# Kernel tuning notes

Measured on AMD Instinct MI355X. Metric: run time of the kernel, lower is better.

## Reference

```python
import jax, jax.numpy as jnp
import numpy as np

OUT = 7          # output_size
SR = 2           # sampling_ratio
IMG = 512.0      # image size (512, 512)
CANON_SCALE = 224.0
CANON_LVL = 4.0
LVL_MIN, LVL_MAX = 2, 6  # strides 4..64


def roi_align_level(feat, rois, scale):
    """torchvision roi_align (aligned=False) for all rois on one level.
    feat: [B,C,H,W], rois: [B,N,4] in image coords. Returns [B,N,C,7,7]."""
    B, C, H, W = feat.shape
    N = rois.shape[1]
    x1 = rois[..., 0] * scale
    y1 = rois[..., 1] * scale
    x2 = rois[..., 2] * scale
    y2 = rois[..., 3] * scale
    roi_w = jnp.maximum(x2 - x1, 1.0)
    roi_h = jnp.maximum(y2 - y1, 1.0)
    bin_w = roi_w / OUT
    bin_h = roi_h / OUT
    # 14 sample coordinates per axis: 7 bins x 2 samples, offset (i+0.5)/2 within bin
    grid = (jnp.arange(OUT, dtype=feat.dtype)[:, None]
            + (jnp.arange(SR, dtype=feat.dtype)[None, :] + 0.5) / SR).reshape(-1)  # [14]
    py = y1[..., None] + grid * bin_h[..., None]   # [B,N,14]
    px = x1[..., None] + grid * bin_w[..., None]   # [B,N,14]
    yy = py[..., :, None]                          # [B,N,14,1]
    xx = px[..., None, :]                          # [B,N,1,14]
    valid = (yy >= -1.0) & (yy <= H) & (xx >= -1.0) & (xx <= W)  # [B,N,14,14]
    y = jnp.clip(yy, 0.0, H - 1)
    x = jnp.clip(xx, 0.0, W - 1)
    y0f = jnp.floor(y)
    x0f = jnp.floor(x)
    ly = y - y0f   # [B,N,14,1]
    lx = x - x0f   # [B,N,1,14]
    y0 = y0f.astype(jnp.int32)
    x0 = x0f.astype(jnp.int32)
    y1i = jnp.minimum(y0 + 1, H - 1)
    x1i = jnp.minimum(x0 + 1, W - 1)

    flat = feat.reshape(B, C, H * W)

    def gather(yi, xi):
        idx = (yi * W + xi).reshape(B, -1)                     # [B, N*14*14]
        g = jax.vmap(lambda f, i: f[:, i])(flat, idx)          # [B, C, N*14*14]
        return g.reshape(B, C, N, SR * OUT, SR * OUT)

    w00 = ((1 - ly) * (1 - lx))[:, None]  # [B,1,N,14,14]
    w01 = ((1 - ly) * lx)[:, None]
    w10 = (ly * (1 - lx))[:, None]
    w11 = (ly * lx)[:, None]
    val = (gather(y0, x0) * w00 + gather(y0, x1i) * w01
           + gather(y1i, x0) * w10 + gather(y1i, x1i) * w11)
    val = val * valid[:, None].astype(feat.dtype)
    # average the SRxSR samples within each bin
    out = val.reshape(B, C, N, OUT, SR, OUT, SR).mean(axis=(4, 6))  # [B,C,N,7,7]
    return out.transpose(0, 2, 1, 3, 4)  # [B,N,C,7,7]


def setup_inputs() -> dict:
    key = jax.random.key(0)
    ks = jax.random.split(key, 6)
    B, C, N = 4, 256, 256
    feats = {}
    for lvl, hw in enumerate([128, 64, 32, 16, 8]):
        feats[f"feat{lvl}"] = jax.random.normal(ks[lvl], (B, C, hw, hw), dtype=jnp.float32)
    # random boxes inside the 512x512 image with x2>x1, y2>y1
    xy = jax.random.uniform(ks[5], (B, N, 2, 2), minval=0.0, maxval=IMG)
    lo = xy.min(axis=2)
    hi = xy.max(axis=2)
    rois = jnp.concatenate([lo, hi], axis=-1)  # [B,N,4] = (x1,y1,x2,y2)
    feats["rois"] = rois
    return feats


def reference(feat0, feat1, feat2, feat3, feat4, rois):
    B, N = rois.shape[0], rois.shape[1]
    feats = [feat0, feat1, feat2, feat3, feat4]
    scales = [0.25, 0.125, 0.0625, 0.03125, 0.015625]  # inferred from 128..8 vs 512
    # FPN level assignment (torchvision LevelMapper)
    area = (rois[..., 2] - rois[..., 0]) * (rois[..., 3] - rois[..., 1])
    lvl = jnp.floor(CANON_LVL + jnp.log2(jnp.sqrt(area) / CANON_SCALE + 1e-6))
    lvl = (jnp.clip(lvl, LVL_MIN, LVL_MAX) - LVL_MIN).astype(jnp.int32)  # [B,N] in 0..4
    # pool every roi on every level, then select its assigned level
    stacked = jnp.stack([roi_align_level(f, rois, s) for f, s in zip(feats, scales)],
                        axis=2)  # [B,N,5,C,7,7]
    sel = jnp.take_along_axis(stacked,
                              lvl[:, :, None, None, None, None].astype(jnp.int32),
                              axis=2)[:, :, 0]  # [B,N,C,7,7]
    B_, N_, C, _, _ = sel.shape
    return sel.reshape(B_ * N_, C, OUT, OUT)
```

## Files before the change

### kernel.cpp

```cpp
#include <hip/hip_runtime.h>

#define OUT 7
#define NB 4
#define NC 256
#define NN 256
#define EPR (NC * OUT * OUT)

typedef float nfloat4 __attribute__((ext_vector_type(4)));

__global__ __launch_bounds__(256) void transpose_cl(
    const float* __restrict__ in, float* __restrict__ outT, int P)
{
    __shared__ float tile[32][33];
    const int p0 = blockIdx.x * 32;
    const int c0 = blockIdx.y * 32;
    const int b  = blockIdx.z;
    const int tx = threadIdx.x;
    const int ty = threadIdx.y;

    const float* src = in + ((size_t)(b * NC + c0 + ty)) * P + p0 + tx * 4;
    nfloat4 v = *(const nfloat4*)src;
    tile[ty][tx * 4 + 0] = v.x;
    tile[ty][tx * 4 + 1] = v.y;
    tile[ty][tx * 4 + 2] = v.z;
    tile[ty][tx * 4 + 3] = v.w;
    __syncthreads();

    nfloat4 w;
    w.x = tile[4 * tx + 0][ty];
    w.y = tile[4 * tx + 1][ty];
    w.z = tile[4 * tx + 2][ty];
    w.w = tile[4 * tx + 3][ty];
    float* dst = outT + ((size_t)b * P + p0 + ty) * NC + c0 + tx * 4;
    *(nfloat4*)dst = w;
}

__global__ __launch_bounds__(256) void msroi_fast(
    const float* __restrict__ T, const float* __restrict__ rois,
    float* __restrict__ out)
{
    const int roi = blockIdx.x;
    const int c   = threadIdx.x;

    __shared__ float s_wyt[14], s_wyb[14], s_wxl[14], s_wxr[14];
    __shared__ int   s_yr0[14], s_yr1[14], s_x0[14], s_x1[14];
    __shared__ int   s_lvl;
    __shared__ __align__(16) float s_out[EPR];

    if (c < 28) {
        const float rx1 = rois[roi * 4 + 0];
        const float ry1 = rois[roi * 4 + 1];
        const float rx2 = rois[roi * 4 + 2];
        const float ry2 = rois[roi * 4 + 3];

        float area = (rx2 - rx1) * (ry2 - ry1);
        float lf = floorf(4.0f + log2f(sqrtf(area) / 224.0f + 1e-6f));
        lf = fminf(fmaxf(lf, 2.0f), 6.0f);
        int lvl = (int)lf - 2;
        if (c == 0) s_lvl = lvl;

        float scale = 1.0f / (float)(4 << lvl);
        int   W     = 128 >> lvl;

        float x1 = rx1 * scale, y1 = ry1 * scale;
        float x2 = rx2 * scale, y2 = ry2 * scale;
        float rw = fmaxf(x2 - x1, 1.0f);
        float rh = fmaxf(y2 - y1, 1.0f);
        float bw = rw / (float)OUT;
        float bh = rh / (float)OUT;

        bool isx = (c >= 14);
        int  g   = isx ? c - 14 : c;
        float gv = ((float)g + 0.5f) * 0.5f;
        float p  = isx ? (x1 + gv * bw) : (y1 + gv * bh);

        float v = (p >= -1.0f && p <= (float)W) ? 1.0f : 0.0f;
        float pc  = fminf(fmaxf(p, 0.0f), (float)(W - 1));
        float p0f = floorf(pc);
        int   p0  = (int)p0f;
        int   p1  = min(p0 + 1, W - 1);
        float l   = pc - p0f;

        if (isx) {
            s_x0[g] = p0; s_x1[g] = p1;
            s_wxl[g] = v * (1.0f - l); s_wxr[g] = v * l;
        } else {
            s_yr0[g] = p0 * W; s_yr1[g] = p1 * W;
            s_wyt[g] = v * (1.0f - l); s_wyb[g] = v * l;
        }
    }
    __syncthreads();

    const int lvl = s_lvl;
    const int W   = 128 >> lvl;
    const int POS = W * W;
    const int off_tab[5] = {0, 16777216, 20971520, 22020096, 22282240};
    const int b = roi >> 8;
    const float* base = T + (size_t)off_tab[lvl] + (size_t)b * POS * NC + c;

    for (int oy = 0; oy < OUT; ++oy) {
        const int gy0 = oy * 2, gy1 = gy0 + 1;
        const float wt0 = s_wyt[gy0], wb0 = s_wyb[gy0];
        const float wt1 = s_wyt[gy1], wb1 = s_wyb[gy1];
        const int r00 = s_yr0[gy0], r01 = s_yr1[gy0];
        const int r10 = s_yr0[gy1], r11 = s_yr1[gy1];
        #pragma unroll
        for (int ox = 0; ox < OUT; ++ox) {
            const int gx0 = ox * 2, gx1 = gx0 + 1;
            const float wl0 = s_wxl[gx0], wr0 = s_wxr[gx0];
            const float wl1 = s_wxl[gx1], wr1 = s_wxr[gx1];
            const int x00 = s_x0[gx0], x01 = s_x1[gx0];
            const int x10 = s_x0[gx1], x11 = s_x1[gx1];

            float acc;
            acc  = wt0 * (wl0 * base[(r00 + x00) << 8] + wr0 * base[(r00 + x01) << 8])
                 + wb0 * (wl0 * base[(r01 + x00) << 8] + wr0 * base[(r01 + x01) << 8]);
            acc += wt0 * (wl1 * base[(r00 + x10) << 8] + wr1 * base[(r00 + x11) << 8])
                 + wb0 * (wl1 * base[(r01 + x10) << 8] + wr1 * base[(r01 + x11) << 8]);
            acc += wt1 * (wl0 * base[(r10 + x00) << 8] + wr0 * base[(r10 + x01) << 8])
                 + wb1 * (wl0 * base[(r11 + x00) << 8] + wr0 * base[(r11 + x01) << 8]);
            acc += wt1 * (wl1 * base[(r10 + x10) << 8] + wr1 * base[(r10 + x11) << 8])
                 + wb1 * (wl1 * base[(r11 + x10) << 8] + wr1 * base[(r11 + x11) << 8]);

            s_out[c * 49 + oy * 7 + ox] = acc * 0.25f;
        }
    }
    __syncthreads();

    float* ob = out + (size_t)roi * EPR;
    #pragma unroll
    for (int k = 0; k < 12; ++k) {
        const int f = (c + (k << 8)) << 2;
        nfloat4 v = *(const nfloat4*)&s_out[f];
        __builtin_nontemporal_store(v, (nfloat4*)&ob[f]);
    }
    if (c < 64) {
        const int f = (c + 3072) << 2;
        nfloat4 v = *(const nfloat4*)&s_out[f];
        __builtin_nontemporal_store(v, (nfloat4*)&ob[f]);
    }
}

__global__ __launch_bounds__(256) void msroi_kernel(
    const float* __restrict__ f0, const float* __restrict__ f1,
    const float* __restrict__ f2, const float* __restrict__ f3,
    const float* __restrict__ f4, const float* __restrict__ rois,
    float* __restrict__ out)
{
    const int roi = blockIdx.y;
    const int tid = threadIdx.x;

    __shared__ float s_wyt[14], s_wyb[14];
    __shared__ float s_wxl[14], s_wxr[14];
    __shared__ int   s_oy0[14], s_oy1[14];
    __shared__ int   s_x0[14],  s_x1[14];
    __shared__ int   s_lvl;

    if (tid < 28) {
        const float rx1 = rois[roi * 4 + 0];
        const float ry1 = rois[roi * 4 + 1];
        const float rx2 = rois[roi * 4 + 2];
        const float ry2 = rois[roi * 4 + 3];

        float area = (rx2 - rx1) * (ry2 - ry1);
        float lf = floorf(4.0f + log2f(sqrtf(area) / 224.0f + 1e-6f));
        lf = fminf(fmaxf(lf, 2.0f), 6.0f);
        int lvl = (int)lf - 2;
        if (tid == 0) s_lvl = lvl;

        float scale = 1.0f / (float)(4 << lvl);
        int   HW    = 128 >> lvl;

        float x1 = rx1 * scale, y1 = ry1 * scale;
        float x2 = rx2 * scale, y2 = ry2 * scale;
        float rw = fmaxf(x2 - x1, 1.0f);
        float rh = fmaxf(y2 - y1, 1.0f);
        float bw = rw / (float)OUT;
        float bh = rh / (float)OUT;

        bool isx = (tid >= 14);
        int  g   = isx ? tid - 14 : tid;
        float gv = ((float)g + 0.5f) * 0.5f;
        float p  = isx ? (x1 + gv * bw) : (y1 + gv * bh);

        float v = (p >= -1.0f && p <= (float)HW) ? 1.0f : 0.0f;
        float pc  = fminf(fmaxf(p, 0.0f), (float)(HW - 1));
        float p0f = floorf(pc);
        int   p0  = (int)p0f;
        int   p1  = min(p0 + 1, HW - 1);
        float l   = pc - p0f;

        if (isx) {
            s_x0[g] = p0; s_x1[g] = p1;
            s_wxl[g] = v * (1.0f - l); s_wxr[g] = v * l;
        } else {
            s_oy0[g] = p0 * HW; s_oy1[g] = p1 * HW;
            s_wyt[g] = v * (1.0f - l); s_wyb[g] = v * l;
        }
    }
    __syncthreads();

    const int lvl = s_lvl;
    const int HW  = 128 >> lvl;
    const int HW2 = HW * HW;
    const float* f = (lvl == 0) ? f0 : (lvl == 1) ? f1 : (lvl == 2) ? f2
                     : (lvl == 3) ? f3 : f4;
    const int b = roi >> 8;

    const int e0 = blockIdx.x * 512 + tid;

    float acc[2];
    #pragma unroll
    for (int k = 0; k < 2; ++k) {
        const int e  = e0 + k * 256;
        const int ec = (e < EPR) ? e : 0;
        const int c  = ec / 49;
        const int s  = ec - 49 * c;
        const int oy = s / 7;
        const int ox = s - 7 * oy;

        const float* fp = f + (size_t)(b * NC + c) * (size_t)HW2;

        float a = 0.0f;
        #pragma unroll
        for (int iy = 0; iy < 2; ++iy) {
            const int gy = oy * 2 + iy;
            const float wt = s_wyt[gy], wb = s_wyb[gy];
            const int   o0 = s_oy0[gy], o1 = s_oy1[gy];
            #pragma unroll
            for (int ix = 0; ix < 2; ++ix) {
                const int gx = ox * 2 + ix;
                const float wl = s_wxl[gx], wr = s_wxr[gx];
                const int   x0 = s_x0[gx],  x1i = s_x1[gx];
                const float v00 = fp[o0 + x0];
                const float v01 = fp[o0 + x1i];
                const float v10 = fp[o1 + x0];
                const float v11 = fp[o1 + x1i];
                a += (wt * wl) * v00 + (wt * wr) * v01
                   + (wb * wl) * v10 + (wb * wr) * v11;
            }
        }
        acc[k] = a * 0.25f;
    }

    #pragma unroll
    for (int k = 0; k < 2; ++k) {
        const int e = e0 + k * 256;
        if (e < EPR)
            __builtin_nontemporal_store(acc[k], &out[(size_t)roi * EPR + e]);
    }
}

extern "C" void kernel_launch(void* const* d_in, const int* in_sizes, int n_in,
                              void* d_out, int out_size, void* d_ws, size_t ws_size,
                              hipStream_t stream) {
    const float* f[5] = {(const float*)d_in[0], (const float*)d_in[1],
                         (const float*)d_in[2], (const float*)d_in[3],
                         (const float*)d_in[4]};
    const float* rois = (const float*)d_in[5];
    float* out = (float*)d_out;

    const size_t need = 22347776ull * 4ull;
    if (ws_size >= need) {
        float* T = (float*)d_ws;
        const int P[5]   = {16384, 4096, 1024, 256, 64};
        const int off[5] = {0, 16777216, 20971520, 22020096, 22282240};
        for (int l = 0; l < 5; ++l) {
            dim3 g(P[l] / 32, NC / 32, NB);
            dim3 blk(8, 32);
            transpose_cl<<<g, blk, 0, stream>>>(f[l], T + off[l], P[l]);
        }
        msroi_fast<<<dim3(NB * NN), dim3(256), 0, stream>>>(T, rois, out);
    } else {
        dim3 grid((EPR + 511) / 512, NB * NN);
        dim3 block(256);
        msroi_kernel<<<grid, block, 0, stream>>>(f[0], f[1], f[2], f[3], f[4],
                                                 rois, out);
    }
}
```

Measured before the change: 200.3 us.

## Fuse per-level transposes into one launch and split ROI pooling across channel chunks

The five per-level channel-last transpose launches are merged into one kernel that finds its level and tile from a flattened block index, removing four launches and the tail gaps between them. The pooling kernel now runs 4 blocks per ROI, each covering 64 channels, with the 49 output bins split across four thread groups. This shrinks shared memory per block from the full 256x49 tile to 64x49 and asks for 6 blocks per CU, to raise occupancy and hide gather latency. In exchange, each block recomputes the ROI sampling tables, and gathers now cover 64 contiguous channels (256 bytes) rather than 256.

```diff
diff --git a/kernel.cpp b/kernel.cpp
--- a/kernel.cpp
+++ b/kernel.cpp
@@ -8,17 +8,31 @@
 
 typedef float nfloat4 __attribute__((ext_vector_type(4)));
 
-__global__ __launch_bounds__(256) void transpose_cl(
-    const float* __restrict__ in, float* __restrict__ outT, int P)
+__global__ __launch_bounds__(256) void transpose_all(
+    const float* __restrict__ f0, const float* __restrict__ f1,
+    const float* __restrict__ f2, const float* __restrict__ f3,
+    const float* __restrict__ f4, float* __restrict__ T)
 {
     __shared__ float tile[32][33];
-    const int p0 = blockIdx.x * 32;
-    const int c0 = blockIdx.y * 32;
-    const int b  = blockIdx.z;
-    const int tx = threadIdx.x;
-    const int ty = threadIdx.y;
-
-    const float* src = in + ((size_t)(b * NC + c0 + ty)) * P + p0 + tx * 4;
+    const int bx = blockIdx.x;
+
+    const float* in; float* outp; int P, t, shp;
+    if (bx < 16384)      { in = f0; outp = T;            P = 16384; t = bx;         shp = 9; }
+    else if (bx < 20480) { in = f1; outp = T + 16777216; P = 4096;  t = bx - 16384; shp = 7; }
+    else if (bx < 21504) { in = f2; outp = T + 20971520; P = 1024;  t = bx - 20480; shp = 5; }
+    else if (bx < 21760) { in = f3; outp = T + 22020096; P = 256;   t = bx - 21504; shp = 3; }
+    else                 { in = f4; outp = T + 22282240; P = 64;    t = bx - 21760; shp = 1; }
+
+    const int pt   = t & ((1 << shp) - 1);
+    const int rest = t >> shp;
+    const int ct   = rest & 7;
+    const int b    = rest >> 3;
+    const int p0   = pt << 5;
+    const int c0   = ct << 5;
+    const int tx   = threadIdx.x & 7;
+    const int ty   = threadIdx.x >> 3;
+
+    const float* src = in + ((size_t)((b << 8) + c0 + ty)) * P + p0 + (tx << 2);
     nfloat4 v = *(const nfloat4*)src;
     tile[ty][tx * 4 + 0] = v.x;
     tile[ty][tx * 4 + 1] = v.y;
@@ -31,23 +45,24 @@
     w.y = tile[4 * tx + 1][ty];
     w.z = tile[4 * tx + 2][ty];
     w.w = tile[4 * tx + 3][ty];
-    float* dst = outT + ((size_t)b * P + p0 + ty) * NC + c0 + tx * 4;
+    float* dst = outp + ((size_t)b * P + p0 + ty) * NC + c0 + (tx << 2);
     *(nfloat4*)dst = w;
 }
 
-__global__ __launch_bounds__(256) void msroi_fast(
+__global__ __launch_bounds__(256, 6) void msroi_fast(
     const float* __restrict__ T, const float* __restrict__ rois,
     float* __restrict__ out)
 {
-    const int roi = blockIdx.x;
-    const int c   = threadIdx.x;
+    const int roi   = blockIdx.y;
+    const int chunk = blockIdx.x;
+    const int tid   = threadIdx.x;
 
     __shared__ float s_wyt[14], s_wyb[14], s_wxl[14], s_wxr[14];
     __shared__ int   s_yr0[14], s_yr1[14], s_x0[14], s_x1[14];
     __shared__ int   s_lvl;
-    __shared__ __align__(16) float s_out[EPR];
-
-    if (c < 28) {
+    __shared__ __align__(16) float s_out[64 * 49];
+
+    if (tid < 28) {
         const float rx1 = rois[roi * 4 + 0];
         const float ry1 = rois[roi * 4 + 1];
         const float rx2 = rois[roi * 4 + 2];
@@ -57,7 +72,7 @@
         float lf = floorf(4.0f + log2f(sqrtf(area) / 224.0f + 1e-6f));
         lf = fminf(fmaxf(lf, 2.0f), 6.0f);
         int lvl = (int)lf - 2;
-        if (c == 0) s_lvl = lvl;
+        if (tid == 0) s_lvl = lvl;
 
         float scale = 1.0f / (float)(4 << lvl);
         int   W     = 128 >> lvl;
@@ -69,8 +84,8 @@
         float bw = rw / (float)OUT;
         float bh = rh / (float)OUT;
 
-        bool isx = (c >= 14);
-        int  g   = isx ? c - 14 : c;
+        bool isx = (tid >= 14);
+        int  g   = isx ? tid - 14 : tid;
         float gv = ((float)g + 0.5f) * 0.5f;
         float p  = isx ? (x1 + gv * bw) : (y1 + gv * bh);
 
@@ -96,48 +111,54 @@
     const int POS = W * W;
     const int off_tab[5] = {0, 16777216, 20971520, 22020096, 22282240};
     const int b = roi >> 8;
-    const float* base = T + (size_t)off_tab[lvl] + (size_t)b * POS * NC + c;
-
-    for (int oy = 0; oy < OUT; ++oy) {
+    const int c = tid & 63;
+    const int q = tid >> 6;
+    const float* base = T + (size_t)off_tab[lvl]
+                          + (size_t)b * POS * NC + (chunk << 6) + c;
+
+    const int pstart = (q * 49) >> 2;
+    const int pend   = ((q + 1) * 49) >> 2;
+
+    for (int pos = pstart; pos < pend; ++pos) {
+        const int oy = pos / 7;
+        const int ox = pos - oy * 7;
         const int gy0 = oy * 2, gy1 = gy0 + 1;
+        const int gx0 = ox * 2, gx1 = gx0 + 1;
+
         const float wt0 = s_wyt[gy0], wb0 = s_wyb[gy0];
         const float wt1 = s_wyt[gy1], wb1 = s_wyb[gy1];
         const int r00 = s_yr0[gy0], r01 = s_yr1[gy0];
         const int r10 = s_yr0[gy1], r11 = s_yr1[gy1];
-        #pragma unroll
-        for (int ox = 0; ox < OUT; ++ox) {
-            const int gx0 = ox * 2, gx1 = gx0 + 1;
-            const float wl0 = s_wxl[gx0], wr0 = s_wxr[gx0];
-            const float wl1 = s_wxl[gx1], wr1 = s_wxr[gx1];
-            const int x00 = s_x0[gx0], x01 = s_x1[gx0];
-            const int x10 = s_x0[gx1], x11 = s_x1[gx1];
-
-            float acc;
-            acc  = wt0 * (wl0 * base[(r00 + x00) << 8] + wr0 * base[(r00 + x01) << 8])
-                 + wb0 * (wl0 * base[(r01 + x00) << 8] + wr0 * base[(r01 + x01) << 8]);
-            acc += wt0 * (wl1 * base[(r00 + x10) << 8] + wr1 * base[(r00 + x11) << 8])
-                 + wb0 * (wl1 * base[(r01 + x10) << 8] + wr1 * base[(r01 + x11) << 8]);
-            acc += wt1 * (wl0 * base[(r10 + x00) << 8] + wr0 * base[(r10 + x01) << 8])
-                 + wb1 * (wl0 * base[(r11 + x00) << 8] + wr0 * base[(r11 + x01) << 8]);
-            acc += wt1 * (wl1 * base[(r10 + x10) << 8] + wr1 * base[(r10 + x11) << 8])
-                 + wb1 * (wl1 * base[(r11 + x10) << 8] + wr1 * base[(r11 + x11) << 8]);
-
-            s_out[c * 49 + oy * 7 + ox] = acc * 0.25f;
-        }
-    }
-    __syncthreads();
-
-    float* ob = out + (size_t)roi * EPR;
+        const float wl0 = s_wxl[gx0], wr0 = s_wxr[gx0];
+        const float wl1 = s_wxl[gx1], wr1 = s_wxr[gx1];
+        const int x00 = s_x0[gx0], x01 = s_x1[gx0];
+        const int x10 = s_x0[gx1], x11 = s_x1[gx1];
+
+        float acc;
+        acc  = wt0 * (wl0 * base[(r00 + x00) << 8] + wr0 * base[(r00 + x01) << 8])
+             + wb0 * (wl0 * base[(r01 + x00) << 8] + wr0 * base[(r01 + x01) << 8]);
+        acc += wt0 * (wl1 * base[(r00 + x10) << 8] + wr1 * base[(r00 + x11) << 8])
+             + wb0 * (wl1 * base[(r01 + x10) << 8] + wr1 * base[(r01 + x11) << 8]);
+        acc += wt1 * (wl0 * base[(r10 + x00) << 8] + wr0 * base[(r10 + x01) << 8])
+             + wb1 * (wl0 * base[(r11 + x00) << 8] + wr0 * base[(r11 + x01) << 8]);
+        acc += wt1 * (wl1 * base[(r10 + x10) << 8] + wr1 * base[(r10 + x11) << 8])
+             + wb1 * (wl1 * base[(r11 + x10) << 8] + wr1 * base[(r11 + x11) << 8]);
+
+        s_out[c * 49 + pos] = acc * 0.25f;
+    }
+    __syncthreads();
+
+    float* ob = out + (size_t)roi * EPR + (chunk << 6) * 49;
     #pragma unroll
-    for (int k = 0; k < 12; ++k) {
-        const int f = (c + (k << 8)) << 2;
-        nfloat4 v = *(const nfloat4*)&s_out[f];
-        __builtin_nontemporal_store(v, (nfloat4*)&ob[f]);
-    }
-    if (c < 64) {
-        const int f = (c + 3072) << 2;
-        nfloat4 v = *(const nfloat4*)&s_out[f];
-        __builtin_nontemporal_store(v, (nfloat4*)&ob[f]);
+    for (int k = 0; k < 3; ++k) {
+        const int i = tid + (k << 8);
+        nfloat4 v = *(const nfloat4*)&s_out[i << 2];
+        __builtin_nontemporal_store(v, (nfloat4*)&ob[i << 2]);
+    }
+    if (tid < 16) {
+        const int i = tid + 768;
+        nfloat4 v = *(const nfloat4*)&s_out[i << 2];
+        __builtin_nontemporal_store(v, (nfloat4*)&ob[i << 2]);
     }
 }
 
@@ -254,27 +275,22 @@
 extern "C" void kernel_launch(void* const* d_in, const int* in_sizes, int n_in,
                               void* d_out, int out_size, void* d_ws, size_t ws_size,
                               hipStream_t stream) {
-    const float* f[5] = {(const float*)d_in[0], (const float*)d_in[1],
-                         (const float*)d_in[2], (const float*)d_in[3],
-                         (const float*)d_in[4]};
+    const float* f0   = (const float*)d_in[0];
+    const float* f1   = (const float*)d_in[1];
+    const float* f2   = (const float*)d_in[2];
+    const float* f3   = (const float*)d_in[3];
+    const float* f4   = (const float*)d_in[4];
     const float* rois = (const float*)d_in[5];
     float* out = (float*)d_out;
 
     const size_t need = 22347776ull * 4ull;
     if (ws_size >= need) {
         float* T = (float*)d_ws;
-        const int P[5]   = {16384, 4096, 1024, 256, 64};
-        const int off[5] = {0, 16777216, 20971520, 22020096, 22282240};
-        for (int l = 0; l < 5; ++l) {
-            dim3 g(P[l] / 32, NC / 32, NB);
-            dim3 blk(8, 32);
-            transpose_cl<<<g, blk, 0, stream>>>(f[l], T + off[l], P[l]);
-        }
-        msroi_fast<<<dim3(NB * NN), dim3(256), 0, stream>>>(T, rois, out);
+        transpose_all<<<dim3(21824), dim3(256), 0, stream>>>(f0, f1, f2, f3, f4, T);
+        msroi_fast<<<dim3(4, NB * NN), dim3(256), 0, stream>>>(T, rois, out);
     } else {
         dim3 grid((EPR + 511) / 512, NB * NN);
         dim3 block(256);
-        msroi_kernel<<<grid, block, 0, stream>>>(f[0], f[1], f[2], f[3], f[4],
-                                                 rois, out);
-    }
-}
+        msroi_kernel<<<grid, block, 0, stream>>>(f0, f1, f2, f3, f4, rois, out);
+    }
+}
```

New measurement: 218.1 us. 1.09x slower.
